# Optimization experiments

Measured on AMD Instinct MI355X. Metric: run time of the kernel, lower is better.

## Reference

```python
import jax, jax.numpy as jnp
import numpy as np

N = 10000      # num_nodes
E = 80000      # num_edges (no self-loops; added in reference like PyG GATConv)
DIN, DH, DOUT = 768, 256, 64
EPS = 1e-16


def _gat_conv(x, src, dst, W, a_src, a_dst, b, heads, out_ch):
    """PyG-style GATConv (concat=True, negative_slope=0.2, eval mode).
    x: [n, in]; src/dst: [e] (self-loops already included); W: [in, heads*out_ch];
    a_src/a_dst: [heads, out_ch]; b: [heads*out_ch]. Returns [n, heads*out_ch]."""
    n = x.shape[0]
    h = (x @ W).reshape(n, heads, out_ch)                 # [n, H, C]
    e = jax.nn.leaky_relu((h * a_src).sum(-1)[src] + (h * a_dst).sum(-1)[dst],
                          negative_slope=0.2)             # [e, H]
    m = jax.ops.segment_max(e, dst, num_segments=n)       # [n, H]
    m = jnp.where(jnp.isfinite(m), m, 0.0)                # guard empty segments
    p = jnp.exp(e - m[dst])                               # [e, H]
    denom = jax.ops.segment_sum(p, dst, num_segments=n)   # [n, H]
    alpha = p / (denom[dst] + EPS)                        # [e, H]
    msg = h[src] * alpha[:, :, None]                      # [e, H, C]  (largest buffer)
    out = jax.ops.segment_sum(msg, dst, num_segments=n)   # [n, H, C]
    return out.reshape(n, heads * out_ch) + b


def setup_inputs() -> dict:
    key = jax.random.key(0)
    ks = jax.random.split(key, 20)

    def lin(k, fan_in, fan_out):
        return jax.random.normal(k, (fan_in, fan_out), jnp.float32) / np.sqrt(fan_in)

    x = jax.random.normal(ks[0], (N, DIN), jnp.float32)
    src = jax.random.randint(ks[1], (E,), 0, N)
    off = jax.random.randint(ks[2], (E,), 1, N)
    dst = (src + off) % N                                  # guarantees no self-loops
    edge_index = jnp.stack([src, dst]).astype(jnp.int64)

    inp = {"x": x, "edge_index": edge_index}
    inp["W1"]  = lin(ks[3], DIN, 8 * DH)
    inp["as1"] = jax.random.normal(ks[4], (8, DH), jnp.float32) / np.sqrt(DH)
    inp["ad1"] = jax.random.normal(ks[5], (8, DH), jnp.float32) / np.sqrt(DH)
    inp["b1"]  = jnp.zeros((8 * DH,), jnp.float32)
    inp["W2"]  = lin(ks[6], 8 * DH, 4 * DH)
    inp["as2"] = jax.random.normal(ks[7], (4, DH), jnp.float32) / np.sqrt(DH)
    inp["ad2"] = jax.random.normal(ks[8], (4, DH), jnp.float32) / np.sqrt(DH)
    inp["b2"]  = jnp.zeros((4 * DH,), jnp.float32)
    inp["W3"]  = lin(ks[9], 4 * DH, DOUT)
    inp["as3"] = jax.random.normal(ks[10], (1, DOUT), jnp.float32) / np.sqrt(DOUT)
    inp["ad3"] = jax.random.normal(ks[11], (1, DOUT), jnp.float32) / np.sqrt(DOUT)
    inp["b3"]  = jnp.zeros((DOUT,), jnp.float32)
    # reasoning MLP: 64 -> 256 -> 128 -> 1
    inp["r1w"] = lin(ks[12], DOUT, DH);      inp["r1b"] = jnp.zeros((DH,), jnp.float32)
    inp["r2w"] = lin(ks[13], DH, DH // 2);   inp["r2b"] = jnp.zeros((DH // 2,), jnp.float32)
    inp["r3w"] = lin(ks[14], DH // 2, 1);    inp["r3b"] = jnp.zeros((1,), jnp.float32)
    return inp


def reference(x, edge_index, W1, as1, ad1, b1, W2, as2, ad2, b2,
              W3, as3, ad3, b3, r1w, r1b, r2w, r2b, r3w, r3b):
    n = x.shape[0]
    loops = jnp.arange(n, dtype=edge_index.dtype)
    src = jnp.concatenate([edge_index[0], loops])
    dst = jnp.concatenate([edge_index[1], loops])
    # dropout layers are identity in eval mode
    x1 = jax.nn.elu(_gat_conv(x,  src, dst, W1, as1, ad1, b1, 8, DH))
    x2 = jax.nn.elu(_gat_conv(x1, src, dst, W2, as2, ad2, b2, 4, DH))
    x3 = _gat_conv(x2, src, dst, W3, as3, ad3, b3, 1, DOUT)
    h = jax.nn.relu(x3 @ r1w + r1b)
    h = jax.nn.relu(h @ r2w + r2b)
    node_scores = h @ r3w + r3b                            # [n, 1]
    return node_scores, x3
```

## Files before the change

### kernel.cpp

```cpp
#include <hip/hip_runtime.h>
#include <stdint.h>

typedef unsigned short u16;
using s16x8 = __attribute__((ext_vector_type(8))) short;
using f32x4 = __attribute__((ext_vector_type(4))) float;
using u16x8 = __attribute__((ext_vector_type(8))) unsigned short;
using u16x4 = __attribute__((ext_vector_type(4))) unsigned short;

#define DEVINL __device__ __forceinline__

DEVINL float b2f(u16 u) { return __uint_as_float(((uint32_t)u) << 16); }
DEVINL u16 f2b(float f) {
  uint32_t x = __float_as_uint(f);
  return (u16)((x + 0x7fffu + ((x >> 16) & 1u)) >> 16);
}
DEVINL float ldf(const void* p, size_t i, int isbf) {
  return isbf ? b2f(((const u16*)p)[i]) : ((const float*)p)[i];
}
DEVINL void stf(void* p, size_t i, int isbf, float v) {
  if (isbf) ((u16*)p)[i] = f2b(v);
  else      ((float*)p)[i] = v;
}

typedef __attribute__((address_space(1))) const void gvoid;
typedef __attribute__((address_space(3))) void lvoid;
DEVINL void gload_lds16(const u16* g, u16* l) {
  __builtin_amdgcn_global_load_lds((gvoid*)g, (lvoid*)l, 16, 0, 0);
}

constexpr int NN = 10000;
constexpr int NE = 80000;
constexpr int NTOT = 90000;

__global__ void detect_kernel(const void* __restrict__ x, int* __restrict__ flag) {
  int lane = threadIdx.x;
  u16 w = ((const u16*)x)[lane * 97 + 13];
  int e = (w >> 7) & 0xFF;
  int sane = (e >= 0x50 && e <= 0x8A) ? 1 : 0;
  unsigned long long b = __ballot(sane);
  if (lane == 0) flag[0] = (__popcll(b) >= 56) ? 1 : 0;
}

__global__ void cvt_kernel(const void* __restrict__ in, u16* __restrict__ out,
                           int n, const int* __restrict__ FLAG) {
  int isbf = *FLAG;
  int i = blockIdx.x * 256 + threadIdx.x;
  if (i >= n) return;
  out[i] = isbf ? ((const u16*)in)[i] : f2b(((const float*)in)[i]);
}

struct TD { const void* in; u16* out; int R, C, t0; };
struct TD5 { TD d[5]; };
__global__ void transpose_all(TD5 td, const int* __restrict__ FLAG) {
  int isbf = *FLAG;
  __shared__ float tile[32][33];
  int t = blockIdx.x;
  int k = 0;
#pragma unroll
  for (int j = 1; j < 5; j++) if (t >= td.d[j].t0) k = j;
  const void* in = td.d[k].in;
  u16* out = td.d[k].out;
  int R = td.d[k].R, C = td.d[k].C;
  int tl = t - td.d[k].t0;
  int tcols = C / 32;
  int bx = (tl % tcols) * 32, by = (tl / tcols) * 32;
  int tx = threadIdx.x, ty = threadIdx.y;
  for (int j = 0; j < 32; j += 8) {
    int r = by + ty + j, c = bx + tx;
    tile[ty + j][tx] = ldf(in, (size_t)r * C + c, isbf);
  }
  __syncthreads();
  for (int j = 0; j < 32; j += 8) {
    int r = bx + ty + j, c = by + tx;
    out[(size_t)r * R + c] = f2b(tile[tx][ty + j]);
  }
}

__global__ void init_kernel(int* __restrict__ deg, float* __restrict__ hz, int nz) {
  int i = blockIdx.x * blockDim.x + threadIdx.x;
  if (i < NN) deg[i] = 1;
  if (i < nz) hz[i] = 0.f;
}

__global__ void count_deg_kernel(const int* __restrict__ ei, int* __restrict__ deg) {
  int e = blockIdx.x * blockDim.x + threadIdx.x;
  if (e < NE) atomicAdd(&deg[ei[NE + e]], 1);
}

__global__ __launch_bounds__(1024) void scan_kernel(const int* __restrict__ deg,
                                                    int* __restrict__ offs,
                                                    int* __restrict__ cursor, int n) {
  __shared__ int wsum[16];
  __shared__ int carry_s;
  int tid = threadIdx.x, lane = tid & 63, wid = tid >> 6;
  if (tid == 0) carry_s = 0;
  __syncthreads();
  for (int base = 0; base < n; base += 1024) {
    int idx = base + tid;
    int v = (idx < n) ? deg[idx] : 0;
    int s = v;
#pragma unroll
    for (int o = 1; o < 64; o <<= 1) { int t = __shfl_up(s, o); if (lane >= o) s += t; }
    if (lane == 63) wsum[wid] = s;
    __syncthreads();
    if (wid == 0) {
      int w = (lane < 16) ? wsum[lane] : 0;
#pragma unroll
      for (int o = 1; o < 16; o <<= 1) { int t = __shfl_up(w, o); if (lane >= o) w += t; }
      if (lane < 16) wsum[lane] = w;
    }
    __syncthreads();
    int inc = s + (wid > 0 ? wsum[wid - 1] : 0) + carry_s;
    if (idx < n) { offs[idx + 1] = inc; cursor[idx] = inc - v; }
    __syncthreads();
    if (tid == 0) carry_s += wsum[15];
    __syncthreads();
  }
  if (tid == 0) offs[0] = 0;
}

__global__ void scatter_kernel(const int* __restrict__ ei, int* __restrict__ cursor,
                               int* __restrict__ csr_src) {
  int e = blockIdx.x * blockDim.x + threadIdx.x;
  if (e >= NTOT) return;
  int s, d;
  if (e < NE) { s = ei[e]; d = ei[NE + e]; }
  else        { s = e - NE; d = s; }
  int pos = atomicAdd(&cursor[d], 1);
  csr_src[pos] = s;
}

template <int BM, int BN, int WM, int WN>
__global__ __launch_bounds__(256) void gemm_kernel(const u16* __restrict__ A,
                                                   const u16* __restrict__ Bt,
                                                   u16* __restrict__ C,
                                                   int M, int K, int N, int nN,
                                                   const void* __restrict__ bias,
                                                   int do_relu,
                                                   const void* __restrict__ asrc,
                                                   const void* __restrict__ adst,
                                                   float* __restrict__ hs,
                                                   float* __restrict__ hd,
                                                   int H, int Cc,
                                                   const int* __restrict__ FLAG) {
  constexpr int BK = 64;
  constexpr int WTM = BM / WM, WTN = BN / WN;
  constexpr int FM = WTM / 16, FN = WTN / 16;
  constexpr int ACH = BM / 32;
  constexpr int BCH = BN / 32;

  __shared__ u16 smem[(BM + BN) * BK];
  u16* lA = smem;
  u16* lB = smem + BM * BK;

  int tid = threadIdx.x;
  int lane = tid & 63, wid = tid >> 6;
  int wm = wid / WN, wn = wid % WN;
  int isbf = (bias || asrc) ? *FLAG : 0;

  int nwg = gridDim.x;
  int q = nwg >> 3, r = nwg & 7;
  int xcd = blockIdx.x & 7, pos = blockIdx.x >> 3;
  int wgid = (xcd < r ? xcd * (q + 1) : r * (q + 1) + (xcd - r) * q) + pos;
  int bm0 = (wgid / nN) * BM, bn0 = (wgid % nN) * BN;

  int srow = lane >> 3;
  int scol = ((lane & 7) ^ (lane >> 3)) << 3;

  f32x4 acc[FM][FN];
#pragma unroll
  for (int m = 0; m < FM; m++)
#pragma unroll
    for (int n = 0; n < FN; n++) acc[m][n] = (f32x4){0.f, 0.f, 0.f, 0.f};

  for (int k0 = 0; k0 < K; k0 += BK) {
#pragma unroll
    for (int i = 0; i < ACH; i++) {
      int c = wid * ACH + i;
      int row = c * 8 + srow;
      int grow = bm0 + row;
      if (grow > M - 1) grow = M - 1;
      gload_lds16(A + (size_t)grow * K + k0 + scol, lA + c * 512);
    }
#pragma unroll
    for (int i = 0; i < BCH; i++) {
      int c = wid * BCH + i;
      int row = c * 8 + srow;
      gload_lds16(Bt + (size_t)(bn0 + row) * K + k0 + scol, lB + c * 512);
    }
    __syncthreads();

    int swz = (lane & 7) << 4;
#pragma unroll
    for (int ks = 0; ks < 2; ks++) {
      int kb = ks * 64 + ((lane >> 4) << 4);
      s16x8 af[FM], bf[FN];
#pragma unroll
      for (int m = 0; m < FM; m++) {
        int row = wm * WTM + m * 16 + (lane & 15);
        af[m] = *(const s16x8*)((const char*)lA + row * 128 + (kb ^ swz));
      }
#pragma unroll
      for (int n = 0; n < FN; n++) {
        int row = wn * WTN + n * 16 + (lane & 15);
        bf[n] = *(const s16x8*)((const char*)lB + row * 128 + (kb ^ swz));
      }
#pragma unroll
      for (int m = 0; m < FM; m++)
#pragma unroll
        for (int n = 0; n < FN; n++)
          acc[m][n] = __builtin_amdgcn_mfma_f32_16x16x32_bf16(af[m], bf[n], acc[m][n], 0, 0, 0);
    }
    __syncthreads();
  }

  u16* lC = smem;
  int r0 = (lane >> 4) * 4;
  int head = hs ? (bn0 / Cc) : 0;
  int part = hs ? ((bn0 % Cc) / WTN + wn) : 0;
  float asv[FN], adv[FN];
  float sa[FM][4], da[FM][4];
  if (hs) {
#pragma unroll
    for (int n = 0; n < FN; n++) {
      int colC = (bn0 % Cc) + wn * WTN + n * 16 + (lane & 15);
      asv[n] = ldf(asrc, (size_t)head * Cc + colC, isbf);
      adv[n] = ldf(adst, (size_t)head * Cc + colC, isbf);
    }
#pragma unroll
    for (int m = 0; m < FM; m++)
#pragma unroll
      for (int rr = 0; rr < 4; rr++) { sa[m][rr] = 0.f; da[m][rr] = 0.f; }
  }
#pragma unroll
  for (int m = 0; m < FM; m++)
#pragma unroll
    for (int n = 0; n < FN; n++)
#pragma unroll
      for (int rr = 0; rr < 4; rr++) {
        int row = wm * WTM + m * 16 + r0 + rr;
        int col = wn * WTN + n * 16 + (lane & 15);
        float v = acc[m][n][rr];
        if (bias) v += ldf(bias, bn0 + col, isbf);
        if (do_relu) v = fmaxf(v, 0.f);
        if (hs) { sa[m][rr] += v * asv[n]; da[m][rr] += v * adv[n]; }
        lC[row * BN + col] = f2b(v);
      }
  if (hs) {
#pragma unroll
    for (int m = 0; m < FM; m++) {
#pragma unroll
      for (int mask = 1; mask < 16; mask <<= 1)
#pragma unroll
        for (int rr = 0; rr < 4; rr++) {
          sa[m][rr] += __shfl_xor(sa[m][rr], mask);
          da[m][rr] += __shfl_xor(da[m][rr], mask);
        }
      if ((lane & 15) == 0) {
#pragma unroll
        for (int rr = 0; rr < 4; rr++) {
          int grow = bm0 + wm * WTM + m * 16 + r0 + rr;
          if (grow < M) {
            hs[((size_t)grow * H + head) * 4 + part] = sa[m][rr];
            hd[((size_t)grow * H + head) * 4 + part] = da[m][rr];
          }
        }
      }
    }
  }
  __syncthreads();
  constexpr int CHUNKS = BM * BN / 2048;
  constexpr int CPR = BN / 8;
#pragma unroll
  for (int j = 0; j < CHUNKS; j++) {
    int idx = j * 256 + tid;
    int row = idx / CPR, colb = (idx % CPR) * 16;
    int grow = bm0 + row;
    if (grow < M) {
      int4 v = *(const int4*)((const char*)lC + idx * 16);
      *(int4*)((char*)C + ((size_t)grow * N + bn0) * 2 + colb) = v;
    }
  }
}

__global__ void softmax_kernel(const int* __restrict__ csr_src, const int* __restrict__ offs,
                               const float* __restrict__ hs, const float* __restrict__ hd,
                               float* __restrict__ alpha, int H, int n) {
  int idx = blockIdx.x * blockDim.x + threadIdx.x;
  if (idx >= n * H) return;
  int i = idx / H, hh = idx % H;
  const float4* hs4 = (const float4*)hs;
  float4 hdp = ((const float4*)hd)[idx];
  float hdv = (hdp.x + hdp.y) + (hdp.z + hdp.w);
  int p0 = offs[i], p1 = offs[i + 1];
  float m = -1e30f;
  for (int p = p0; p < p1; ++p) {
    float4 hp = hs4[(size_t)csr_src[p] * H + hh];
    float e = (hp.x + hp.y) + (hp.z + hp.w) + hdv;
    e = e > 0.f ? e : 0.2f * e;
    alpha[(size_t)p * H + hh] = e;
    m = fmaxf(m, e);
  }
  float den = 0.f;
  for (int p = p0; p < p1; ++p) {
    float pe = __expf(alpha[(size_t)p * H + hh] - m);
    alpha[(size_t)p * H + hh] = pe;
    den += pe;
  }
  float inv = 1.f / (den + 1e-16f);
  for (int p = p0; p < p1; ++p) alpha[(size_t)p * H + hh] *= inv;
}

template <int HC, int VPT, int TPB>
__global__ __launch_bounds__(TPB) void aggregate_kernel(
    const u16* __restrict__ h, const float* __restrict__ alpha,
    const int* __restrict__ csr_src, const int* __restrict__ offs,
    const void* __restrict__ bias, u16* __restrict__ outb, void* __restrict__ outv,
    int H, int C, int do_elu, const int* __restrict__ FLAG) {
  int isbf = *FLAG;
  int i = blockIdx.x;
  int t = threadIdx.x;
  int c0 = t * VPT;
  int head = c0 / C;
  float acc[VPT];
#pragma unroll
  for (int j = 0; j < VPT; j++) acc[j] = 0.f;
  int p0 = offs[i], p1 = offs[i + 1];
  int p = p0;
  for (; p + 2 <= p1; p += 2) {
    int s0 = csr_src[p], s1 = csr_src[p + 1];
    float a0 = alpha[(size_t)p * H + head];
    float a1 = alpha[(size_t)(p + 1) * H + head];
    const u16* h0 = h + (size_t)s0 * HC + c0;
    const u16* h1 = h + (size_t)s1 * HC + c0;
    if constexpr (VPT == 8) {
      u16x8 v0 = *(const u16x8*)h0, v1 = *(const u16x8*)h1;
#pragma unroll
      for (int j = 0; j < 8; j++) acc[j] += a0 * b2f(v0[j]) + a1 * b2f(v1[j]);
    } else if constexpr (VPT == 4) {
      u16x4 v0 = *(const u16x4*)h0, v1 = *(const u16x4*)h1;
#pragma unroll
      for (int j = 0; j < 4; j++) acc[j] += a0 * b2f(v0[j]) + a1 * b2f(v1[j]);
    } else {
      acc[0] += a0 * b2f(h0[0]) + a1 * b2f(h1[0]);
    }
  }
  if (p < p1) {
    int s0 = csr_src[p];
    float a0 = alpha[(size_t)p * H + head];
    const u16* h0 = h + (size_t)s0 * HC + c0;
    if constexpr (VPT == 8) {
      u16x8 v0 = *(const u16x8*)h0;
#pragma unroll
      for (int j = 0; j < 8; j++) acc[j] += a0 * b2f(v0[j]);
    } else if constexpr (VPT == 4) {
      u16x4 v0 = *(const u16x4*)h0;
#pragma unroll
      for (int j = 0; j < 4; j++) acc[j] += a0 * b2f(v0[j]);
    } else {
      acc[0] += a0 * b2f(h0[0]);
    }
  }
  float r[VPT];
#pragma unroll
  for (int j = 0; j < VPT; j++) {
    r[j] = acc[j] + ldf(bias, c0 + j, isbf);
    if (do_elu) r[j] = r[j] > 0.f ? r[j] : expm1f(r[j]);
  }
  if (outb) {
    if constexpr (VPT == 8) {
      u16x8 o;
#pragma unroll
      for (int j = 0; j < 8; j++) o[j] = f2b(r[j]);
      *(u16x8*)(outb + (size_t)i * HC + c0) = o;
    } else if constexpr (VPT == 4) {
      u16x4 o;
#pragma unroll
      for (int j = 0; j < 4; j++) o[j] = f2b(r[j]);
      *(u16x4*)(outb + (size_t)i * HC + c0) = o;
    } else {
      outb[(size_t)i * HC + c0] = f2b(r[0]);
    }
  }
  if (outv) {
#pragma unroll
    for (int j = 0; j < VPT; j++)
      stf(outv, (size_t)10000 + (size_t)i * HC + c0 + j, isbf, r[j]);
  }
}

__global__ __launch_bounds__(256) void dot128_kernel(const u16* __restrict__ h2,
                                                     const void* __restrict__ r3w,
                                                     const void* __restrict__ r3b,
                                                     void* __restrict__ scores,
                                                     const int* __restrict__ FLAG) {
  int isbf = *FLAG;
  int wid = threadIdx.x >> 6, lane = threadIdx.x & 63;
  int i = blockIdx.x * 4 + wid;
  if (i >= NN) return;
  const u16* hp = h2 + (size_t)i * 128;
  float v = b2f(hp[lane]) * ldf(r3w, lane, isbf) +
            b2f(hp[lane + 64]) * ldf(r3w, lane + 64, isbf);
  for (int o = 32; o; o >>= 1) v += __shfl_down(v, o);
  if (lane == 0) stf(scores, i, isbf, v + ldf(r3b, 0, isbf));
}

extern "C" void kernel_launch(void* const* d_in, const int* in_sizes, int n_in,
                              void* d_out, int out_size, void* d_ws, size_t ws_size,
                              hipStream_t stream) {
  const void* x   = d_in[0];
  const int* ei   = (const int*)d_in[1];
  const void* W1  = d_in[2];
  const void* as1 = d_in[3];
  const void* ad1 = d_in[4];
  const void* b1  = d_in[5];
  const void* W2  = d_in[6];
  const void* as2 = d_in[7];
  const void* ad2 = d_in[8];
  const void* b2  = d_in[9];
  const void* W3  = d_in[10];
  const void* as3 = d_in[11];
  const void* ad3 = d_in[12];
  const void* b3  = d_in[13];
  const void* r1w = d_in[14];
  const void* r1b = d_in[15];
  const void* r2w = d_in[16];
  const void* r2b = d_in[17];
  const void* r3w = d_in[18];
  const void* r3b = d_in[19];

  char* ws = (char*)d_ws;
  size_t o = 0;
  auto alloc = [&](size_t bytes) { void* p = ws + o; o += (bytes + 255) & ~(size_t)255; return p; };
  u16* XC     = (u16*)alloc((size_t)NN * 768 * 2);
  u16* W1T    = (u16*)alloc((size_t)2048 * 768 * 2);
  u16* W2T    = (u16*)alloc((size_t)1024 * 2048 * 2);
  u16* W3T    = (u16*)alloc((size_t)64 * 1024 * 2);
  u16* R1T    = (u16*)alloc((size_t)256 * 64 * 2);
  u16* R2T    = (u16*)alloc((size_t)128 * 256 * 2);
  u16* Hbuf   = (u16*)alloc((size_t)NN * 2048 * 2);
  u16* Xbuf   = (u16*)alloc((size_t)NN * 2048 * 2);
  u16* X3B    = (u16*)alloc((size_t)NN * 64 * 2);
  u16* H1B    = (u16*)alloc((size_t)NN * 256 * 2);
  u16* H2B    = (u16*)alloc((size_t)NN * 128 * 2);
  float* HZ   = (float*)alloc((size_t)NN * 104 * 4);
  float* HS1  = HZ;
  float* HD1  = HZ + (size_t)NN * 32;
  float* HS2  = HZ + (size_t)NN * 64;
  float* HD2  = HZ + (size_t)NN * 80;
  float* HS3  = HZ + (size_t)NN * 96;
  float* HD3  = HZ + (size_t)NN * 100;
  int* DEG    = (int*)alloc((size_t)NN * 4);
  int* OFFS   = (int*)alloc((size_t)(NN + 1) * 4);
  int* CURSOR = (int*)alloc((size_t)NN * 4);
  int* CSR    = (int*)alloc((size_t)NTOT * 4);
  float* ALPHA = (float*)alloc((size_t)NTOT * 8 * 4);
  int* FLAG   = (int*)alloc(256);

  detect_kernel<<<1, 64, 0, stream>>>(x, FLAG);
  cvt_kernel<<<(NN * 768 + 255) / 256, 256, 0, stream>>>(x, XC, NN * 768, FLAG);

  TD5 td;
  td.d[0] = {W1,  W1T, 768, 2048, 0};
  td.d[1] = {W2,  W2T, 2048, 1024, 0};
  td.d[2] = {W3,  W3T, 1024, 64, 0};
  td.d[3] = {r1w, R1T, 64, 256, 0};
  td.d[4] = {r2w, R2T, 256, 128, 0};
  int cum = 0;
  for (int k = 0; k < 5; k++) {
    td.d[k].t0 = cum;
    cum += (td.d[k].R / 32) * (td.d[k].C / 32);
  }
  transpose_all<<<cum, dim3(32, 8), 0, stream>>>(td, FLAG);

  init_kernel<<<(NN * 104 + 255) / 256, 256, 0, stream>>>(DEG, HZ, NN * 104);
  count_deg_kernel<<<(NE + 255) / 256, 256, 0, stream>>>(ei, DEG);
  scan_kernel<<<1, 1024, 0, stream>>>(DEG, OFFS, CURSOR, NN);
  scatter_kernel<<<(NTOT + 255) / 256, 256, 0, stream>>>(ei, CURSOR, CSR);

  const int MT = (NN + 127) / 128;
  const int MT64 = (NN + 63) / 64;

  gemm_kernel<64, 128, 2, 2><<<MT64 * 16, 256, 0, stream>>>(
      XC, W1T, Hbuf, NN, 768, 2048, 16, nullptr, 0, as1, ad1, HS1, HD1, 8, 256, FLAG);
  softmax_kernel<<<(NN * 8 + 255) / 256, 256, 0, stream>>>(CSR, OFFS, HS1, HD1, ALPHA, 8, NN);
  aggregate_kernel<2048, 8, 256><<<NN, 256, 0, stream>>>(Hbuf, ALPHA, CSR, OFFS, b1, Xbuf, nullptr, 8, 256, 1, FLAG);

  gemm_kernel<64, 128, 2, 2><<<MT64 * 8, 256, 0, stream>>>(
      Xbuf, W2T, Hbuf, NN, 2048, 1024, 8, nullptr, 0, as2, ad2, HS2, HD2, 4, 256, FLAG);
  softmax_kernel<<<(NN * 4 + 255) / 256, 256, 0, stream>>>(CSR, OFFS, HS2, HD2, ALPHA, 4, NN);
  aggregate_kernel<1024, 4, 256><<<NN, 256, 0, stream>>>(Hbuf, ALPHA, CSR, OFFS, b2, Xbuf, nullptr, 4, 256, 1, FLAG);

  gemm_kernel<128, 64, 4, 1><<<MT, 256, 0, stream>>>(
      Xbuf, W3T, Hbuf, NN, 1024, 64, 1, nullptr, 0, as3, ad3, HS3, HD3, 1, 64, FLAG);
  softmax_kernel<<<(NN + 255) / 256, 256, 0, stream>>>(CSR, OFFS, HS3, HD3, ALPHA, 1, NN);
  aggregate_kernel<64, 1, 64><<<NN, 64, 0, stream>>>(Hbuf, ALPHA, CSR, OFFS, b3, X3B, d_out, 1, 64, 0, FLAG);

  gemm_kernel<64, 64, 2, 2><<<MT64 * 4, 256, 0, stream>>>(
      X3B, R1T, H1B, NN, 64, 256, 4, r1b, 1, nullptr, nullptr, nullptr, nullptr, 0, 0, FLAG);
  gemm_kernel<64, 64, 2, 2><<<MT64 * 2, 256, 0, stream>>>(
      H1B, R2T, H2B, NN, 256, 128, 2, r2b, 1, nullptr, nullptr, nullptr, nullptr, 0, 0, FLAG);
  dot128_kernel<<<(NN + 3) / 4, 256, 0, stream>>>(H2B, r3w, r3b, d_out, FLAG);
}
```

Measured before the change: 376.2 us.

## Fuse edge softmax into aggregation and fold final dot into MLP GEMM epilogue

Removes the separate softmax kernel and the per-edge ALPHA buffer. Each aggregation block now computes the per-head max and denominator with warp reductions, then recomputes normalized attention weights chunk by chunk into shared memory. The final 128-wide dot product is folded into the second MLP GEMM's attention-score epilogue, which writes partial sums that a tiny scores kernel adds up, so that GEMM no longer stores its output. This trades extra recomputation of gathered hs loads and block barriers for fewer launches and less global memory traffic.

After: 344.3 us. 8.5% less time.

```diff
diff --git a/kernel.cpp b/kernel.cpp
--- a/kernel.cpp
+++ b/kernel.cpp
@@ -268,115 +268,146 @@
       }
     }
   }
-  __syncthreads();
-  constexpr int CHUNKS = BM * BN / 2048;
-  constexpr int CPR = BN / 8;
-#pragma unroll
-  for (int j = 0; j < CHUNKS; j++) {
-    int idx = j * 256 + tid;
-    int row = idx / CPR, colb = (idx % CPR) * 16;
-    int grow = bm0 + row;
-    if (grow < M) {
-      int4 v = *(const int4*)((const char*)lC + idx * 16);
-      *(int4*)((char*)C + ((size_t)grow * N + bn0) * 2 + colb) = v;
-    }
-  }
-}
-
-__global__ void softmax_kernel(const int* __restrict__ csr_src, const int* __restrict__ offs,
-                               const float* __restrict__ hs, const float* __restrict__ hd,
-                               float* __restrict__ alpha, int H, int n) {
-  int idx = blockIdx.x * blockDim.x + threadIdx.x;
-  if (idx >= n * H) return;
-  int i = idx / H, hh = idx % H;
-  const float4* hs4 = (const float4*)hs;
-  float4 hdp = ((const float4*)hd)[idx];
-  float hdv = (hdp.x + hdp.y) + (hdp.z + hdp.w);
-  int p0 = offs[i], p1 = offs[i + 1];
-  float m = -1e30f;
-  for (int p = p0; p < p1; ++p) {
-    float4 hp = hs4[(size_t)csr_src[p] * H + hh];
-    float e = (hp.x + hp.y) + (hp.z + hp.w) + hdv;
-    e = e > 0.f ? e : 0.2f * e;
-    alpha[(size_t)p * H + hh] = e;
-    m = fmaxf(m, e);
-  }
-  float den = 0.f;
-  for (int p = p0; p < p1; ++p) {
-    float pe = __expf(alpha[(size_t)p * H + hh] - m);
-    alpha[(size_t)p * H + hh] = pe;
-    den += pe;
-  }
-  float inv = 1.f / (den + 1e-16f);
-  for (int p = p0; p < p1; ++p) alpha[(size_t)p * H + hh] *= inv;
-}
-
-template <int HC, int VPT, int TPB>
-__global__ __launch_bounds__(TPB) void aggregate_kernel(
-    const u16* __restrict__ h, const float* __restrict__ alpha,
+  if (C) {
+    __syncthreads();
+    constexpr int CHUNKS = BM * BN / 2048;
+    constexpr int CPR = BN / 8;
+#pragma unroll
+    for (int j = 0; j < CHUNKS; j++) {
+      int idx = j * 256 + tid;
+      int row = idx / CPR, colb = (idx % CPR) * 16;
+      int grow = bm0 + row;
+      if (grow < M) {
+        int4 v = *(const int4*)((const char*)lC + idx * 16);
+        *(int4*)((char*)C + ((size_t)grow * N + bn0) * 2 + colb) = v;
+      }
+    }
+  }
+}
+
+template <int HC, int VPT, int TPB, int H>
+__global__ __launch_bounds__(TPB) void agg_fused_kernel(
+    const u16* __restrict__ h, const float* __restrict__ hs, const float* __restrict__ hd,
     const int* __restrict__ csr_src, const int* __restrict__ offs,
     const void* __restrict__ bias, u16* __restrict__ outb, void* __restrict__ outv,
-    int H, int C, int do_elu, const int* __restrict__ FLAG) {
+    int do_elu, const int* __restrict__ FLAG) {
+  constexpr int C = HC / H;
+  constexpr int CH = 64;
   int isbf = *FLAG;
   int i = blockIdx.x;
   int t = threadIdx.x;
+  int p0 = offs[i], p1 = offs[i + 1];
+  __shared__ float m_s[H], inv_s[H], hd_s[H];
+  __shared__ float lalpha[CH * H];
+  __shared__ int lsrc[CH];
+  const float4* hs4 = (const float4*)hs;
+
+  if (t < H) {
+    float4 qd = ((const float4*)hd)[(size_t)i * H + t];
+    hd_s[t] = (qd.x + qd.y) + (qd.z + qd.w);
+  }
+  __syncthreads();
+
+  int hh = (t >> 5) % H, j = t & 31;
+  bool crew = (t < H * 32);
+  if (crew) {
+    float hdv = hd_s[hh];
+    float mm = -1e30f;
+    for (int p = p0 + j; p < p1; p += 32) {
+      float4 qv = hs4[(size_t)csr_src[p] * H + hh];
+      float e = (qv.x + qv.y) + (qv.z + qv.w) + hdv;
+      e = e > 0.f ? e : 0.2f * e;
+      mm = fmaxf(mm, e);
+    }
+#pragma unroll
+    for (int msk = 16; msk; msk >>= 1) mm = fmaxf(mm, __shfl_xor(mm, msk));
+    float dd = 0.f;
+    for (int p = p0 + j; p < p1; p += 32) {
+      float4 qv = hs4[(size_t)csr_src[p] * H + hh];
+      float e = (qv.x + qv.y) + (qv.z + qv.w) + hdv;
+      e = e > 0.f ? e : 0.2f * e;
+      dd += __expf(e - mm);
+    }
+#pragma unroll
+    for (int msk = 16; msk; msk >>= 1) dd += __shfl_xor(dd, msk);
+    if (j == 0) { m_s[hh] = mm; inv_s[hh] = 1.f / (dd + 1e-16f); }
+  }
+
   int c0 = t * VPT;
   int head = c0 / C;
   float acc[VPT];
 #pragma unroll
-  for (int j = 0; j < VPT; j++) acc[j] = 0.f;
-  int p0 = offs[i], p1 = offs[i + 1];
-  int p = p0;
-  for (; p + 2 <= p1; p += 2) {
-    int s0 = csr_src[p], s1 = csr_src[p + 1];
-    float a0 = alpha[(size_t)p * H + head];
-    float a1 = alpha[(size_t)(p + 1) * H + head];
-    const u16* h0 = h + (size_t)s0 * HC + c0;
-    const u16* h1 = h + (size_t)s1 * HC + c0;
-    if constexpr (VPT == 8) {
-      u16x8 v0 = *(const u16x8*)h0, v1 = *(const u16x8*)h1;
-#pragma unroll
-      for (int j = 0; j < 8; j++) acc[j] += a0 * b2f(v0[j]) + a1 * b2f(v1[j]);
-    } else if constexpr (VPT == 4) {
-      u16x4 v0 = *(const u16x4*)h0, v1 = *(const u16x4*)h1;
-#pragma unroll
-      for (int j = 0; j < 4; j++) acc[j] += a0 * b2f(v0[j]) + a1 * b2f(v1[j]);
-    } else {
-      acc[0] += a0 * b2f(h0[0]) + a1 * b2f(h1[0]);
-    }
-  }
-  if (p < p1) {
-    int s0 = csr_src[p];
-    float a0 = alpha[(size_t)p * H + head];
-    const u16* h0 = h + (size_t)s0 * HC + c0;
-    if constexpr (VPT == 8) {
-      u16x8 v0 = *(const u16x8*)h0;
-#pragma unroll
-      for (int j = 0; j < 8; j++) acc[j] += a0 * b2f(v0[j]);
-    } else if constexpr (VPT == 4) {
-      u16x4 v0 = *(const u16x4*)h0;
-#pragma unroll
-      for (int j = 0; j < 4; j++) acc[j] += a0 * b2f(v0[j]);
-    } else {
-      acc[0] += a0 * b2f(h0[0]);
-    }
-  }
+  for (int v = 0; v < VPT; v++) acc[v] = 0.f;
+
+  for (int base = p0; base < p1; base += CH) {
+    int cend = base + CH < p1 ? base + CH : p1;
+    __syncthreads();
+    if (crew) {
+      float hdv = hd_s[hh];
+      float mmv = m_s[hh], inv = inv_s[hh];
+      for (int p = base + j; p < cend; p += 32) {
+        float4 qv = hs4[(size_t)csr_src[p] * H + hh];
+        float e = (qv.x + qv.y) + (qv.z + qv.w) + hdv;
+        e = e > 0.f ? e : 0.2f * e;
+        lalpha[(p - base) * H + hh] = __expf(e - mmv) * inv;
+      }
+    }
+    if (t < cend - base) lsrc[t] = csr_src[base + t];
+    __syncthreads();
+
+    int p = base;
+    for (; p + 2 <= cend; p += 2) {
+      int s0 = lsrc[p - base], s1 = lsrc[p - base + 1];
+      float a0 = lalpha[(p - base) * H + head];
+      float a1 = lalpha[(p - base + 1) * H + head];
+      const u16* h0 = h + (size_t)s0 * HC + c0;
+      const u16* h1 = h + (size_t)s1 * HC + c0;
+      if constexpr (VPT == 8) {
+        u16x8 v0 = *(const u16x8*)h0, v1 = *(const u16x8*)h1;
+#pragma unroll
+        for (int v = 0; v < 8; v++) acc[v] += a0 * b2f(v0[v]) + a1 * b2f(v1[v]);
+      } else if constexpr (VPT == 4) {
+        u16x4 v0 = *(const u16x4*)h0, v1 = *(const u16x4*)h1;
+#pragma unroll
+        for (int v = 0; v < 4; v++) acc[v] += a0 * b2f(v0[v]) + a1 * b2f(v1[v]);
+      } else {
+        acc[0] += a0 * b2f(h0[0]) + a1 * b2f(h1[0]);
+      }
+    }
+    if (p < cend) {
+      int s0 = lsrc[p - base];
+      float a0 = lalpha[(p - base) * H + head];
+      const u16* h0 = h + (size_t)s0 * HC + c0;
+      if constexpr (VPT == 8) {
+        u16x8 v0 = *(const u16x8*)h0;
+#pragma unroll
+        for (int v = 0; v < 8; v++) acc[v] += a0 * b2f(v0[v]);
+      } else if constexpr (VPT == 4) {
+        u16x4 v0 = *(const u16x4*)h0;
+#pragma unroll
+        for (int v = 0; v < 4; v++) acc[v] += a0 * b2f(v0[v]);
+      } else {
+        acc[0] += a0 * b2f(h0[0]);
+      }
+    }
+  }
+
   float r[VPT];
 #pragma unroll
-  for (int j = 0; j < VPT; j++) {
-    r[j] = acc[j] + ldf(bias, c0 + j, isbf);
-    if (do_elu) r[j] = r[j] > 0.f ? r[j] : expm1f(r[j]);
+  for (int v = 0; v < VPT; v++) {
+    r[v] = acc[v] + ldf(bias, c0 + v, isbf);
+    if (do_elu) r[v] = r[v] > 0.f ? r[v] : expm1f(r[v]);
   }
   if (outb) {
     if constexpr (VPT == 8) {
       u16x8 o;
 #pragma unroll
-      for (int j = 0; j < 8; j++) o[j] = f2b(r[j]);
+      for (int v = 0; v < 8; v++) o[v] = f2b(r[v]);
       *(u16x8*)(outb + (size_t)i * HC + c0) = o;
     } else if constexpr (VPT == 4) {
       u16x4 o;
 #pragma unroll
-      for (int j = 0; j < 4; j++) o[j] = f2b(r[j]);
+      for (int v = 0; v < 4; v++) o[v] = f2b(r[v]);
       *(u16x4*)(outb + (size_t)i * HC + c0) = o;
     } else {
       outb[(size_t)i * HC + c0] = f2b(r[0]);
@@ -384,25 +415,18 @@
   }
   if (outv) {
 #pragma unroll
-    for (int j = 0; j < VPT; j++)
-      stf(outv, (size_t)10000 + (size_t)i * HC + c0 + j, isbf, r[j]);
-  }
-}
-
-__global__ __launch_bounds__(256) void dot128_kernel(const u16* __restrict__ h2,
-                                                     const void* __restrict__ r3w,
-                                                     const void* __restrict__ r3b,
-                                                     void* __restrict__ scores,
-                                                     const int* __restrict__ FLAG) {
+    for (int v = 0; v < VPT; v++)
+      stf(outv, (size_t)10000 + (size_t)i * HC + c0 + v, isbf, r[v]);
+  }
+}
+
+__global__ void scores_kernel(const float* __restrict__ sc, const void* __restrict__ r3b,
+                              void* __restrict__ scores, const int* __restrict__ FLAG) {
   int isbf = *FLAG;
-  int wid = threadIdx.x >> 6, lane = threadIdx.x & 63;
-  int i = blockIdx.x * 4 + wid;
+  int i = blockIdx.x * 256 + threadIdx.x;
   if (i >= NN) return;
-  const u16* hp = h2 + (size_t)i * 128;
-  float v = b2f(hp[lane]) * ldf(r3w, lane, isbf) +
-            b2f(hp[lane + 64]) * ldf(r3w, lane + 64, isbf);
-  for (int o = 32; o; o >>= 1) v += __shfl_down(v, o);
-  if (lane == 0) stf(scores, i, isbf, v + ldf(r3b, 0, isbf));
+  float4 q = ((const float4*)sc)[i];
+  stf(scores, i, isbf, (q.x + q.y) + (q.z + q.w) + ldf(r3b, 0, isbf));
 }
 
 extern "C" void kernel_launch(void* const* d_in, const int* in_sizes, int n_in,
@@ -442,19 +466,19 @@
   u16* Xbuf   = (u16*)alloc((size_t)NN * 2048 * 2);
   u16* X3B    = (u16*)alloc((size_t)NN * 64 * 2);
   u16* H1B    = (u16*)alloc((size_t)NN * 256 * 2);
-  u16* H2B    = (u16*)alloc((size_t)NN * 128 * 2);
-  float* HZ   = (float*)alloc((size_t)NN * 104 * 4);
+  float* HZ   = (float*)alloc((size_t)NN * 112 * 4);
   float* HS1  = HZ;
   float* HD1  = HZ + (size_t)NN * 32;
   float* HS2  = HZ + (size_t)NN * 64;
   float* HD2  = HZ + (size_t)NN * 80;
   float* HS3  = HZ + (size_t)NN * 96;
   float* HD3  = HZ + (size_t)NN * 100;
+  float* SC   = HZ + (size_t)NN * 104;
+  float* SD   = HZ + (size_t)NN * 108;
   int* DEG    = (int*)alloc((size_t)NN * 4);
   int* OFFS   = (int*)alloc((size_t)(NN + 1) * 4);
   int* CURSOR = (int*)alloc((size_t)NN * 4);
   int* CSR    = (int*)alloc((size_t)NTOT * 4);
-  float* ALPHA = (float*)alloc((size_t)NTOT * 8 * 4);
   int* FLAG   = (int*)alloc(256);
 
   detect_kernel<<<1, 64, 0, stream>>>(x, FLAG);
@@ -473,7 +497,7 @@
   }
   transpose_all<<<cum, dim3(32, 8), 0, stream>>>(td, FLAG);
 
-  init_kernel<<<(NN * 104 + 255) / 256, 256, 0, stream>>>(DEG, HZ, NN * 104);
+  init_kernel<<<(NN * 112 + 255) / 256, 256, 0, stream>>>(DEG, HZ, NN * 112);
   count_deg_kernel<<<(NE + 255) / 256, 256, 0, stream>>>(ei, DEG);
   scan_kernel<<<1, 1024, 0, stream>>>(DEG, OFFS, CURSOR, NN);
   scatter_kernel<<<(NTOT + 255) / 256, 256, 0, stream>>>(ei, CURSOR, CSR);
@@ -483,22 +507,22 @@
 
   gemm_kernel<64, 128, 2, 2><<<MT64 * 16, 256, 0, stream>>>(
       XC, W1T, Hbuf, NN, 768, 2048, 16, nullptr, 0, as1, ad1, HS1, HD1, 8, 256, FLAG);
-  softmax_kernel<<<(NN * 8 + 255) / 256, 256, 0, stream>>>(CSR, OFFS, HS1, HD1, ALPHA, 8, NN);
-  aggregate_kernel<2048, 8, 256><<<NN, 256, 0, stream>>>(Hbuf, ALPHA, CSR, OFFS, b1, Xbuf, nullptr, 8, 256, 1, FLAG);
+  agg_fused_kernel<2048, 8, 256, 8><<<NN, 256, 0, stream>>>(
+      Hbuf, HS1, HD1, CSR, OFFS, b1, Xbuf, nullptr, 1, FLAG);
 
   gemm_kernel<64, 128, 2, 2><<<MT64 * 8, 256, 0, stream>>>(
       Xbuf, W2T, Hbuf, NN, 2048, 1024, 8, nullptr, 0, as2, ad2, HS2, HD2, 4, 256, FLAG);
-  softmax_kernel<<<(NN * 4 + 255) / 256, 256, 0, stream>>>(CSR, OFFS, HS2, HD2, ALPHA, 4, NN);
-  aggregate_kernel<1024, 4, 256><<<NN, 256, 0, stream>>>(Hbuf, ALPHA, CSR, OFFS, b2, Xbuf, nullptr, 4, 256, 1, FLAG);
+  agg_fused_kernel<1024, 4, 256, 4><<<NN, 256, 0, stream>>>(
+      Hbuf, HS2, HD2, CSR, OFFS, b2, Xbuf, nullptr, 1, FLAG);
 
   gemm_kernel<128, 64, 4, 1><<<MT, 256, 0, stream>>>(
       Xbuf, W3T, Hbuf, NN, 1024, 64, 1, nullptr, 0, as3, ad3, HS3, HD3, 1, 64, FLAG);
-  softmax_kernel<<<(NN + 255) / 256, 256, 0, stream>>>(CSR, OFFS, HS3, HD3, ALPHA, 1, NN);
-  aggregate_kernel<64, 1, 64><<<NN, 64, 0, stream>>>(Hbuf, ALPHA, CSR, OFFS, b3, X3B, d_out, 1, 64, 0, FLAG);
+  agg_fused_kernel<64, 1, 64, 1><<<NN, 64, 0, stream>>>(
+      Hbuf, HS3, HD3, CSR, OFFS, b3, X3B, d_out, 0, FLAG);
 
   gemm_kernel<64, 64, 2, 2><<<MT64 * 4, 256, 0, stream>>>(
       X3B, R1T, H1B, NN, 64, 256, 4, r1b, 1, nullptr, nullptr, nullptr, nullptr, 0, 0, FLAG);
   gemm_kernel<64, 64, 2, 2><<<MT64 * 2, 256, 0, stream>>>(
-      H1B, R2T, H2B, NN, 256, 128, 2, r2b, 1, nullptr, nullptr, nullptr, nullptr, 0, 0, FLAG);
-  dot128_kernel<<<(NN + 3) / 4, 256, 0, stream>>>(H2B, r3w, r3b, d_out, FLAG);
-}
+      H1B, R2T, nullptr, NN, 256, 128, 2, r2b, 1, r3w, r3w, SC, SD, 1, 128, FLAG);
+  scores_kernel<<<(NN + 255) / 256, 256, 0, stream>>>(SC, r3b, d_out, FLAG);
+}
```
